# Kernel optimization log

Measured on AMD Instinct MI355X. Metric: run time of the kernel, lower is better.

The kernel has to match this reference:

```python
import jax, jax.numpy as jnp
import numpy as np

N = 8192
E = 131072
NODE_DIM = 128
HIDDEN_DIM = 256


def setup_inputs() -> dict:
    key = jax.random.key(0)
    k1, k2, k3 = jax.random.split(key, 3)
    x = jax.random.normal(k1, (N, NODE_DIM), dtype=jnp.float32)
    edge_index = jax.random.randint(k2, (2, E), 0, N, dtype=jnp.int64)
    # nn.Linear(node_dim, hidden_dim, bias=False): weight [hidden_dim, node_dim]
    W = jax.random.normal(k3, (HIDDEN_DIM, NODE_DIM), dtype=jnp.float32) * (1.0 / np.sqrt(NODE_DIM))
    return {"x": x, "edge_index": edge_index, "W": W}


def reference(x, edge_index, W):
    num_nodes = x.shape[0]
    src, tgt = edge_index[0], edge_index[1]
    # Dense adjacency: A[src, tgt] = 1 (set semantics, duplicates collapse)
    A = jnp.zeros((num_nodes, num_nodes), dtype=x.dtype).at[src, tgt].set(1.0)
    A_tilde = A + jnp.eye(num_nodes, dtype=x.dtype)
    D = A_tilde.sum(axis=1)
    D_inv_sqrt = D ** -0.5
    # D_tilde @ A_tilde @ D_tilde == row/col scaling of A_tilde
    A_hat = D_inv_sqrt[:, None] * A_tilde * D_inv_sqrt[None, :]
    out = A_hat @ x            # [N, node_dim]
    out = out @ W.T            # [N, hidden_dim]
    return out
```

## Files before the change

### kernel.cpp

```cpp
#include <hip/hip_runtime.h>

#define N_NODES 8192
#define NODE_DIM 128
#define HIDDEN_DIM 256
#define WORDS_PER_ROW 256
#define CAP 96

typedef __attribute__((ext_vector_type(8))) short bf16x8;
typedef __attribute__((ext_vector_type(4))) float f32x4;

static __device__ __forceinline__ unsigned short f2bf(float f) {
    unsigned u = __builtin_bit_cast(unsigned, f);
    unsigned r = u + 0x7fffu + ((u >> 16) & 1u);
    return (unsigned short)(r >> 16);
}
static __device__ __forceinline__ float bf2f(unsigned short h) {
    unsigned u = ((unsigned)h) << 16;
    return __builtin_bit_cast(float, u);
}

__global__ void dedupe_kernel(const int* __restrict__ e,
                              unsigned int* __restrict__ bitmask,
                              unsigned int* __restrict__ deg,
                              int* __restrict__ rowlist,
                              const float* __restrict__ W,
                              unsigned short* __restrict__ wh,
                              unsigned short* __restrict__ wl,
                              int E, int nEdgeBlocks) {
    if ((int)blockIdx.x < nEdgeBlocks) {
        int idx = blockIdx.x * 256 + threadIdx.x;
        if (idx >= E) return;
        int s = e[idx];
        int t = e[E + idx];
        unsigned int w = (unsigned int)s * WORDS_PER_ROW + ((unsigned int)t >> 5);
        unsigned int m = 1u << (t & 31);
        unsigned int old = atomicOr(&bitmask[w], m);
        if (!(old & m)) {
            unsigned int p = atomicAdd(&deg[s], 1u);
            if (p < CAP) rowlist[(size_t)s * CAP + p] = t;
        }
    } else {
        int t = (blockIdx.x - nEdgeBlocks) * 256 + threadIdx.x;
        if (t >= HIDDEN_DIM * NODE_DIM / 4) return;
        float4 v = ((const float4*)W)[t];
        ushort4 h, l;
        h.x = f2bf(v.x); l.x = f2bf(v.x - bf2f(h.x));
        h.y = f2bf(v.y); l.y = f2bf(v.y - bf2f(h.y));
        h.z = f2bf(v.z); l.z = f2bf(v.z - bf2f(h.z));
        h.w = f2bf(v.w); l.w = f2bf(v.w - bf2f(h.w));
        ((ushort4*)wh)[t] = h;
        ((ushort4*)wl)[t] = l;
    }
}

__global__ __launch_bounds__(256)
void aggregate_kernel(const int* __restrict__ rowlist,
                      const unsigned int* __restrict__ deg,
                      const float* __restrict__ x,
                      unsigned short* __restrict__ yh,
                      unsigned short* __restrict__ yl) {
    __shared__ int   cols[CAP];
    __shared__ float djs[CAP];
    __shared__ float part[NODE_DIM];
    int i   = blockIdx.x;
    int tid = threadIdx.x;
    int n   = (int)deg[i];
    if (n > CAP) n = CAP;
    if (tid < n) {
        int c = rowlist[(size_t)i * CAP + tid];
        cols[tid] = c;
        djs[tid]  = rsqrtf((float)deg[c] + 1.0f);
    }
    __syncthreads();

    int g = tid >> 7;
    int d = tid & 127;
    float acc = 0.0f;
    for (int k = g; k < n; k += 2) {
        acc += djs[k] * x[(size_t)cols[k] * NODE_DIM + d];
    }
    if (g == 0) part[d] = acc;
    __syncthreads();
    if (g == 1) {
        float di = rsqrtf((float)n + 1.0f);
        float v  = di * (di * x[(size_t)i * NODE_DIM + d] + part[d] + acc);
        unsigned short h = f2bf(v);
        unsigned short l = f2bf(v - bf2f(h));
        yh[(size_t)i * NODE_DIM + d] = h;
        yl[(size_t)i * NODE_DIM + d] = l;
    }
}

__global__ __launch_bounds__(256)
void gemm_kernel(const unsigned short* __restrict__ Yh,
                 const unsigned short* __restrict__ Yl,
                 const unsigned short* __restrict__ Wh,
                 const unsigned short* __restrict__ Wl,
                 float* __restrict__ out) {
    int tid  = threadIdx.x;
    int wave = tid >> 6;
    int lane = tid & 63;
    int quad = lane >> 4;
    int l16  = lane & 15;
    int m0   = blockIdx.y * 64;
    int hcol = blockIdx.x * 64 + wave * 16 + l16;

    const unsigned short* wh_p = Wh + (size_t)hcol * NODE_DIM + quad * 8;
    const unsigned short* wl_p = Wl + (size_t)hcol * NODE_DIM + quad * 8;
    const unsigned short* yh_p = Yh + (size_t)(m0 + l16) * NODE_DIM + quad * 8;
    const unsigned short* yl_p = Yl + (size_t)(m0 + l16) * NODE_DIM + quad * 8;

    f32x4 acc[4] = {{0,0,0,0},{0,0,0,0},{0,0,0,0},{0,0,0,0}};
#pragma unroll
    for (int ks = 0; ks < 4; ++ks) {
        int k = ks * 32;
        bf16x8 bh = *(const bf16x8*)(wh_p + k);
        bf16x8 bl = *(const bf16x8*)(wl_p + k);
#pragma unroll
        for (int mt = 0; mt < 4; ++mt) {
            bf16x8 ah = *(const bf16x8*)(yh_p + k + mt * 16 * NODE_DIM);
            bf16x8 al = *(const bf16x8*)(yl_p + k + mt * 16 * NODE_DIM);
            acc[mt] = __builtin_amdgcn_mfma_f32_16x16x32_bf16(ah, bh, acc[mt], 0, 0, 0);
            acc[mt] = __builtin_amdgcn_mfma_f32_16x16x32_bf16(ah, bl, acc[mt], 0, 0, 0);
            acc[mt] = __builtin_amdgcn_mfma_f32_16x16x32_bf16(al, bh, acc[mt], 0, 0, 0);
        }
    }

#pragma unroll
    for (int mt = 0; mt < 4; ++mt) {
#pragma unroll
        for (int r = 0; r < 4; ++r) {
            out[(size_t)(m0 + mt * 16 + quad * 4 + r) * HIDDEN_DIM + hcol] = acc[mt][r];
        }
    }
}

extern "C" void kernel_launch(void* const* d_in, const int* in_sizes, int n_in,
                              void* d_out, int out_size, void* d_ws, size_t ws_size,
                              hipStream_t stream) {
    const float* x = (const float*)d_in[0];
    const int*   e = (const int*)d_in[1];
    const float* W = (const float*)d_in[2];
    float*       out = (float*)d_out;
    int E = in_sizes[1] / 2;

    unsigned int*   bitmask = (unsigned int*)d_ws;
    unsigned int*   deg     = bitmask + (size_t)N_NODES * WORDS_PER_ROW;
    int*            rowlist = (int*)(deg + N_NODES);
    unsigned short* yh      = (unsigned short*)(rowlist + (size_t)N_NODES * CAP);
    unsigned short* yl      = yh + (size_t)N_NODES * NODE_DIM;
    unsigned short* wh      = yl + (size_t)N_NODES * NODE_DIM;
    unsigned short* wl      = wh + (size_t)HIDDEN_DIM * NODE_DIM;

    size_t clear_bytes = ((size_t)N_NODES * WORDS_PER_ROW + N_NODES) * sizeof(unsigned int);
    hipMemsetAsync(d_ws, 0, clear_bytes, stream);

    int nEdgeBlocks = (E + 255) / 256;
    int nWBlocks    = (HIDDEN_DIM * NODE_DIM / 4 + 255) / 256;
    dedupe_kernel<<<nEdgeBlocks + nWBlocks, 256, 0, stream>>>(e, bitmask, deg, rowlist,
                                                              W, wh, wl, E, nEdgeBlocks);
    aggregate_kernel<<<N_NODES, 256, 0, stream>>>(rowlist, deg, x, yh, yl);
    gemm_kernel<<<dim3(HIDDEN_DIM / 64, N_NODES / 64), 256, 0, stream>>>(yh, yl, wh, wl, out);
}
```

Baseline: 104.9 us.

## Fuse neighbor aggregation and GEMM into one kernel with LDS-staged rows

Merges the aggregation and split-bf16 GEMM kernels into one kernel that processes 16 rows per block. Each 32-thread team aggregates one row using float4 gathers and writes the bf16 hi/lo result to LDS, and the MFMA GEMM then reads it from LDS. This drops the global round trip of the intermediate Y and one kernel launch. In exchange, W is re-read from global/L2 by every block, and the per-row aggregation uses fewer threads per row.

```diff
diff --git a/kernel.cpp b/kernel.cpp
--- a/kernel.cpp
+++ b/kernel.cpp
@@ -5,6 +5,8 @@
 #define HIDDEN_DIM 256
 #define WORDS_PER_ROW 256
 #define CAP 96
+#define RPB 16
+#define YLD 136
 
 typedef __attribute__((ext_vector_type(8))) short bf16x8;
 typedef __attribute__((ext_vector_type(4))) float f32x4;
@@ -53,84 +55,106 @@
     }
 }
 
-__global__ __launch_bounds__(256)
-void aggregate_kernel(const int* __restrict__ rowlist,
-                      const unsigned int* __restrict__ deg,
-                      const float* __restrict__ x,
-                      unsigned short* __restrict__ yh,
-                      unsigned short* __restrict__ yl) {
-    __shared__ int   cols[CAP];
-    __shared__ float djs[CAP];
-    __shared__ float part[NODE_DIM];
-    int i   = blockIdx.x;
+__global__ __launch_bounds__(512)
+void fused_agg_gemm(const int* __restrict__ rowlist,
+                    const unsigned int* __restrict__ deg,
+                    const float* __restrict__ x,
+                    const unsigned short* __restrict__ Wh,
+                    const unsigned short* __restrict__ Wl,
+                    float* __restrict__ out) {
+    __shared__ int            nrow[RPB];
+    __shared__ float          sdi[RPB];
+    __shared__ int            cols[RPB][CAP];
+    __shared__ float          djs[RPB][CAP];
+    __shared__ unsigned short Yh[RPB][YLD];
+    __shared__ unsigned short Yl[RPB][YLD];
+
     int tid = threadIdx.x;
-    int n   = (int)deg[i];
-    if (n > CAP) n = CAP;
-    if (tid < n) {
-        int c = rowlist[(size_t)i * CAP + tid];
-        cols[tid] = c;
-        djs[tid]  = rsqrtf((float)deg[c] + 1.0f);
+    int m0  = blockIdx.x * RPB;
+
+    if (tid < RPB) {
+        unsigned int dg = deg[m0 + tid];
+        int n = (int)dg; if (n > CAP) n = CAP;
+        nrow[tid] = n;
+        sdi[tid]  = rsqrtf((float)dg + 1.0f);
     }
     __syncthreads();
 
-    int g = tid >> 7;
-    int d = tid & 127;
-    float acc = 0.0f;
-    for (int k = g; k < n; k += 2) {
-        acc += djs[k] * x[(size_t)cols[k] * NODE_DIM + d];
-    }
-    if (g == 0) part[d] = acc;
-    __syncthreads();
-    if (g == 1) {
-        float di = rsqrtf((float)n + 1.0f);
-        float v  = di * (di * x[(size_t)i * NODE_DIM + d] + part[d] + acc);
-        unsigned short h = f2bf(v);
-        unsigned short l = f2bf(v - bf2f(h));
-        yh[(size_t)i * NODE_DIM + d] = h;
-        yl[(size_t)i * NODE_DIM + d] = l;
-    }
-}
-
-__global__ __launch_bounds__(256)
-void gemm_kernel(const unsigned short* __restrict__ Yh,
-                 const unsigned short* __restrict__ Yl,
-                 const unsigned short* __restrict__ Wh,
-                 const unsigned short* __restrict__ Wl,
-                 float* __restrict__ out) {
-    int tid  = threadIdx.x;
-    int wave = tid >> 6;
-    int lane = tid & 63;
-    int quad = lane >> 4;
-    int l16  = lane & 15;
-    int m0   = blockIdx.y * 64;
-    int hcol = blockIdx.x * 64 + wave * 16 + l16;
-
-    const unsigned short* wh_p = Wh + (size_t)hcol * NODE_DIM + quad * 8;
-    const unsigned short* wl_p = Wl + (size_t)hcol * NODE_DIM + quad * 8;
-    const unsigned short* yh_p = Yh + (size_t)(m0 + l16) * NODE_DIM + quad * 8;
-    const unsigned short* yl_p = Yl + (size_t)(m0 + l16) * NODE_DIM + quad * 8;
-
-    f32x4 acc[4] = {{0,0,0,0},{0,0,0,0},{0,0,0,0},{0,0,0,0}};
-#pragma unroll
-    for (int ks = 0; ks < 4; ++ks) {
-        int k = ks * 32;
-        bf16x8 bh = *(const bf16x8*)(wh_p + k);
-        bf16x8 bl = *(const bf16x8*)(wl_p + k);
-#pragma unroll
-        for (int mt = 0; mt < 4; ++mt) {
-            bf16x8 ah = *(const bf16x8*)(yh_p + k + mt * 16 * NODE_DIM);
-            bf16x8 al = *(const bf16x8*)(yl_p + k + mt * 16 * NODE_DIM);
-            acc[mt] = __builtin_amdgcn_mfma_f32_16x16x32_bf16(ah, bh, acc[mt], 0, 0, 0);
-            acc[mt] = __builtin_amdgcn_mfma_f32_16x16x32_bf16(ah, bl, acc[mt], 0, 0, 0);
-            acc[mt] = __builtin_amdgcn_mfma_f32_16x16x32_bf16(al, bh, acc[mt], 0, 0, 0);
+    for (int e = tid; e < RPB * CAP; e += 512) {
+        int r = e / CAP, k = e - r * CAP;
+        if (k < nrow[r]) {
+            int c = rowlist[(size_t)(m0 + r) * CAP + k];
+            cols[r][k] = c;
+            djs[r][k]  = rsqrtf((float)deg[c] + 1.0f);
         }
     }
+    __syncthreads();
 
+    {
+        int team = tid >> 5;
+        int l4   = tid & 31;
+        const float4* x4 = (const float4*)x;
+        int   n    = nrow[team];
+        float di   = sdi[team];
+        float4 self = x4[(size_t)(m0 + team) * 32 + l4];
+        float ax = 0.f, ay = 0.f, az = 0.f, aw = 0.f;
+        int k = 0;
+        for (; k + 2 <= n; k += 2) {
+            float  d0 = djs[team][k];
+            float  d1 = djs[team][k + 1];
+            float4 v0 = x4[(size_t)cols[team][k]     * 32 + l4];
+            float4 v1 = x4[(size_t)cols[team][k + 1] * 32 + l4];
+            ax += d0 * v0.x + d1 * v1.x;
+            ay += d0 * v0.y + d1 * v1.y;
+            az += d0 * v0.z + d1 * v1.z;
+            aw += d0 * v0.w + d1 * v1.w;
+        }
+        if (k < n) {
+            float  d0 = djs[team][k];
+            float4 v0 = x4[(size_t)cols[team][k] * 32 + l4];
+            ax += d0 * v0.x; ay += d0 * v0.y; az += d0 * v0.z; aw += d0 * v0.w;
+        }
+        float vx = di * (di * self.x + ax);
+        float vy = di * (di * self.y + ay);
+        float vz = di * (di * self.z + az);
+        float vw = di * (di * self.w + aw);
+        ushort4 h, l;
+        h.x = f2bf(vx); l.x = f2bf(vx - bf2f(h.x));
+        h.y = f2bf(vy); l.y = f2bf(vy - bf2f(h.y));
+        h.z = f2bf(vz); l.z = f2bf(vz - bf2f(h.z));
+        h.w = f2bf(vw); l.w = f2bf(vw - bf2f(h.w));
+        *(ushort4*)&Yh[team][l4 * 4] = h;
+        *(ushort4*)&Yl[team][l4 * 4] = l;
+    }
+    __syncthreads();
+
+    {
+        int wave = tid >> 6;
+        int lane = tid & 63;
+        int quad = lane >> 4;
+        int l16  = lane & 15;
+
+        f32x4 acc[2] = {{0,0,0,0},{0,0,0,0}};
 #pragma unroll
-    for (int mt = 0; mt < 4; ++mt) {
+        for (int ks = 0; ks < 4; ++ks) {
+            bf16x8 ah = *(const bf16x8*)&Yh[l16][ks * 32 + quad * 8];
+            bf16x8 al = *(const bf16x8*)&Yl[l16][ks * 32 + quad * 8];
 #pragma unroll
-        for (int r = 0; r < 4; ++r) {
-            out[(size_t)(m0 + mt * 16 + quad * 4 + r) * HIDDEN_DIM + hcol] = acc[mt][r];
+            for (int ct = 0; ct < 2; ++ct) {
+                int hcol = wave * 32 + ct * 16 + l16;
+                bf16x8 bh = *(const bf16x8*)(Wh + (size_t)hcol * NODE_DIM + ks * 32 + quad * 8);
+                bf16x8 bl = *(const bf16x8*)(Wl + (size_t)hcol * NODE_DIM + ks * 32 + quad * 8);
+                acc[ct] = __builtin_amdgcn_mfma_f32_16x16x32_bf16(ah, bh, acc[ct], 0, 0, 0);
+                acc[ct] = __builtin_amdgcn_mfma_f32_16x16x32_bf16(ah, bl, acc[ct], 0, 0, 0);
+                acc[ct] = __builtin_amdgcn_mfma_f32_16x16x32_bf16(al, bh, acc[ct], 0, 0, 0);
+            }
+        }
+#pragma unroll
+        for (int ct = 0; ct < 2; ++ct) {
+#pragma unroll
+            for (int r = 0; r < 4; ++r) {
+                out[(size_t)(m0 + quad * 4 + r) * HIDDEN_DIM + wave * 32 + ct * 16 + l16] = acc[ct][r];
+            }
         }
     }
 }
@@ -147,9 +171,7 @@
     unsigned int*   bitmask = (unsigned int*)d_ws;
     unsigned int*   deg     = bitmask + (size_t)N_NODES * WORDS_PER_ROW;
     int*            rowlist = (int*)(deg + N_NODES);
-    unsigned short* yh      = (unsigned short*)(rowlist + (size_t)N_NODES * CAP);
-    unsigned short* yl      = yh + (size_t)N_NODES * NODE_DIM;
-    unsigned short* wh      = yl + (size_t)N_NODES * NODE_DIM;
+    unsigned short* wh      = (unsigned short*)(rowlist + (size_t)N_NODES * CAP);
     unsigned short* wl      = wh + (size_t)HIDDEN_DIM * NODE_DIM;
 
     size_t clear_bytes = ((size_t)N_NODES * WORDS_PER_ROW + N_NODES) * sizeof(unsigned int);
@@ -159,6 +181,5 @@
     int nWBlocks    = (HIDDEN_DIM * NODE_DIM / 4 + 255) / 256;
     dedupe_kernel<<<nEdgeBlocks + nWBlocks, 256, 0, stream>>>(e, bitmask, deg, rowlist,
                                                               W, wh, wl, E, nEdgeBlocks);
-    aggregate_kernel<<<N_NODES, 256, 0, stream>>>(rowlist, deg, x, yh, yl);
-    gemm_kernel<<<dim3(HIDDEN_DIM / 64, N_NODES / 64), 256, 0, stream>>>(yh, yl, wh, wl, out);
+    fused_agg_gemm<<<N_NODES / RPB, 512, 0, stream>>>(rowlist, deg, x, wh, wl, out);
 }
```

Measured after the change: 91.21 us. 13.0% less time.
